# Performance work log

Hardware: AMD Instinct MI355X
Metric: run time of the kernel (lower is better)

Reference implementation:

```python
import jax, jax.numpy as jnp
import numpy as np

N = 600          # total nodes in episode
C = 5            # num_classes_output
Q = 16           # query_size
NQ = C * Q       # 80 query nodes (last rows)
F_IN = (1024, 1024)
EMB = (128, 128)
FE = 256         # final_embed_size
K = 3            # conv1d kernel
ST = 1           # conv1d stride
CAT = sum(EMB) + C            # 261
FC = FE + (FE - K) // ST + 1  # 510


def _edges():
    per = (N - NQ) // C
    labels = np.concatenate([np.repeat(np.arange(C), per), np.repeat(np.arange(C), Q)]).astype(np.int64)
    temp = labels.copy()
    temp[-NQ:] = -np.arange(1, NQ + 1)  # queries get unique pseudo-labels
    same = temp[:, None] == temp[None, :]
    eye = np.eye(N, dtype=bool)
    in_src, in_dst = np.nonzero(same & ~eye)        # in-class edges
    cr_src, cr_dst = np.nonzero(~same)              # cross-class edges
    q = np.arange(N - NQ, N); s = np.arange(N - NQ)
    a = np.repeat(q, s.size); b = np.tile(s, q.size)
    fin_src = np.concatenate([a, b]); fin_dst = np.concatenate([b, a])  # query<->support pooling
    f = lambda x: jnp.asarray(x, jnp.int32)
    return f(labels), f(in_src), f(in_dst), f(cr_src), f(cr_dst), f(fin_src), f(fin_dst)


def gcn(x, W, b, src, dst):
    # PyG GCNConv: add self-loops, D^-1/2 (A+I) D^-1/2 (X W) + b
    n = x.shape[0]
    loop = jnp.arange(n, dtype=src.dtype)
    s = jnp.concatenate([src, loop]); d = jnp.concatenate([dst, loop])
    deg = jax.ops.segment_sum(jnp.ones(s.shape, x.dtype), d, num_segments=n)
    dinv = jax.lax.rsqrt(deg)  # deg >= 1 (self-loops)
    norm = dinv[s] * dinv[d]
    h = x @ W
    return jax.ops.segment_sum(h[s] * norm[:, None], d, num_segments=n) + b


def gatv2(x, Wl, bl, Wr, br, att, b, src, dst):
    # PyG GATv2Conv (heads=1): e_ji = a . leaky_relu(hl[j] + hr[i]); out_i = sum_j softmax(e)_ji * hl[j]
    n = x.shape[0]
    loop = jnp.arange(n, dtype=src.dtype)
    s = jnp.concatenate([src, loop]); d = jnp.concatenate([dst, loop])
    hl = x @ Wl + bl
    hr = x @ Wr + br
    e = jax.nn.leaky_relu(hl[s] + hr[d], negative_slope=0.2) @ att  # [E]
    m = jax.ops.segment_max(e, d, num_segments=n)
    ex = jnp.exp(e - m[d])
    den = jax.ops.segment_sum(ex, d, num_segments=n)
    alpha = ex / den[d]
    return jax.ops.segment_sum(alpha[:, None] * hl[s], d, num_segments=n) + b


def setup_inputs() -> dict:
    key = jax.random.key(0)
    ks = jax.random.split(key, 12)
    labels, in_src, in_dst, cr_src, cr_dst, fin_src, fin_dst = _edges()
    p = lambda k, shp: jax.random.normal(k, shp, jnp.float32) * 0.05
    z = lambda shp: jnp.zeros(shp, jnp.float32)
    return {
        'features0': jax.random.normal(ks[0], (N, F_IN[0]), jnp.float32),
        'features1': jax.random.normal(ks[1], (N, F_IN[1]), jnp.float32),
        'labels': labels,
        'in_src': in_src, 'in_dst': in_dst,
        'cr_src': cr_src, 'cr_dst': cr_dst,
        'fin_src': fin_src, 'fin_dst': fin_dst,
        'W_f0': p(ks[2], (F_IN[0], EMB[0])), 'b_f0': z((EMB[0],)),
        'W_f1': p(ks[3], (F_IN[1], EMB[1])), 'b_f1': z((EMB[1],)),
        'W_in': p(ks[4], (CAT, FE)), 'b_in': z((FE,)),
        'Wl': p(ks[5], (CAT, FE)), 'bl': z((FE,)),
        'Wr': p(ks[6], (CAT, FE)), 'br': z((FE,)),
        'att_a': p(ks[7], (FE,)), 'b_gat': z((FE,)),
        'conv_w': p(ks[8], (1, 1, K)), 'conv_b': z((1,)),
        'W_lab': p(ks[9], (FC, C)), 'b_lab': z((C,)),
    }


def reference(features0, features1, labels, in_src, in_dst, cr_src, cr_dst, fin_src, fin_dst,
              W_f0, b_f0, W_f1, b_f1, W_in, b_in, Wl, bl, Wr, br, att_a, b_gat,
              conv_w, conv_b, W_lab, b_lab):
    ns = N - NQ
    one_hot = jnp.concatenate([
        jax.nn.one_hot(labels[:ns], C, dtype=jnp.float32),
        jnp.full((NQ, C), 1.0 / C, jnp.float32)], axis=0)
    # per-feature GCN embeddings (dropout = identity at inference)
    h0 = jax.nn.leaky_relu(gcn(features0, W_f0, b_f0, in_src, in_dst))
    h1 = jax.nn.leaky_relu(gcn(features1, W_f1, b_f1, in_src, in_dst))
    cated = jnp.concatenate([h0, h1, one_hot], axis=-1)  # [N, 261]
    gcn_emb = jax.nn.leaky_relu(gcn(cated, W_in, b_in, in_src, in_dst))          # [N, FE]
    gat_emb = jax.nn.elu(gatv2(cated, Wl, bl, Wr, br, att_a, b_gat, cr_src, cr_dst))  # [N, FE]
    conv = jax.lax.conv_general_dilated(gat_emb[:, None, :], conv_w, (ST,), 'VALID',
                                        dimension_numbers=('NCH', 'OIH', 'NCH'))
    gat_emb = jax.nn.sigmoid(conv[:, 0, :] + conv_b[0])  # [N, FE-K+1]
    fc = jnp.concatenate([gcn_emb, gat_emb], axis=-1)    # [N, FC]
    return gcn(fc, W_lab, b_lab, fin_src, fin_dst)       # [N, C]
```

## Files before the change

### kernel.cpp

```cpp
#include <hip/hip_runtime.h>

#define N_NODES 600
#define NSUP    520
#define NQ      80
#define C_CLS   5
#define PER     104
#define F_IN    1024
#define EMBF    128
#define FE      256
#define CATD    261
#define CST     264
#define FCD     510
#define CONV_OUT 254
#define R85     85

__global__ __launch_bounds__(1024) void k1_k(const float* __restrict__ f0,
                                             const float* __restrict__ f1,
                                             const float* __restrict__ Wf0,
                                             const float* __restrict__ Wf1,
                                             const float* __restrict__ bf0,
                                             const float* __restrict__ bf1,
                                             const float* __restrict__ Win,
                                             const float* __restrict__ Wl,
                                             const float* __restrict__ Wr,
                                             float* __restrict__ embp,
                                             float* __restrict__ xrow85,
                                             int* __restrict__ ctr) {
    __shared__ float xs[F_IN];
    __shared__ float part[1024];
    const int gb = blockIdx.x, t = threadIdx.x;
    if (gb == 0 && t == 0) *ctr = 0;
    if (gb < 40) {
        const int js  = gb & 3;
        const int c   = (gb >> 2) % C_CLS;
        const int set = gb / 20;
        const float* X = set ? f1 : f0;
        const float* W = set ? Wf1 : Wf0;
        const float* p = X + (size_t)(c * PER + js * 26) * F_IN + t;
        float acc = 0.f;
        for (int b = 0; b < 2; ++b) {
            float wv[13];
#pragma unroll
            for (int i = 0; i < 13; ++i) wv[i] = p[(size_t)(b * 13 + i) * F_IN];
#pragma unroll
            for (int i = 0; i < 13; ++i) acc += wv[i];
        }
        xs[t] = acc;
        __syncthreads();
        const int col = t & 127, kseg = t >> 7;
        const float* Wp = W + (size_t)(kseg * 128) * EMBF + col;
        const float* xp = xs + kseg * 128;
        float pacc = 0.f;
        for (int b = 0; b < 4; ++b) {
            float wv[32];
#pragma unroll
            for (int i = 0; i < 32; ++i) wv[i] = Wp[(size_t)(b * 32 + i) * EMBF];
#pragma unroll
            for (int i = 0; i < 32; ++i) pacc += xp[b * 32 + i] * wv[i];
        }
        part[t] = pacc;
        __syncthreads();
        if (t < 128) {
            float s = 0.f;
#pragma unroll
            for (int j = 0; j < 8; ++j) s += part[t + 128 * j];
            embp[((size_t)(set * 4 + js) * C_CLS + c) * EMBF + t] = s;
        }
    } else if (gb < 200) {
        const int idx = gb - 40, q = idx >> 1, set = idx & 1;
        const float* X = set ? f1 : f0;
        const float* W = set ? Wf1 : Wf0;
        if (t < 256) ((float4*)xs)[t] = ((const float4*)(X + (size_t)(NSUP + q) * F_IN))[t];
        __syncthreads();
        const int col = t & 127, kseg = t >> 7;
        const float* Wp = W + (size_t)(kseg * 128) * EMBF + col;
        const float* xp = xs + kseg * 128;
        float acc = 0.f;
        for (int b = 0; b < 4; ++b) {
            float wv[32];
#pragma unroll
            for (int i = 0; i < 32; ++i) wv[i] = Wp[(size_t)(b * 32 + i) * EMBF];
#pragma unroll
            for (int i = 0; i < 32; ++i) acc += xp[b * 32 + i] * wv[i];
        }
        part[t] = acc;
        __syncthreads();
        const int r = C_CLS + q;
        if (t < 128) {
            float s = 0.f;
#pragma unroll
            for (int j = 0; j < 8; ++j) s += part[t + 128 * j];
            s += (set ? bf1[t] : bf0[t]);
            s = s > 0.f ? s : 0.01f * s;
            xrow85[r * CST + set * EMBF + t] = s;
        }
        if (set == 0 && t < C_CLS) xrow85[r * CST + FE + t] = 0.2f;
    } else {
        const int wt = (gb - 200) * 1024 + t;
        float acc = 0.f;
        for (int i = wt; i < 16704 * 3; i += 16384) {
            const float4* p;
            int j = i;
            if (j < 16704) p = (const float4*)Win + j;
            else if ((j -= 16704) < 16704) p = (const float4*)Wl + j;
            else { j -= 16704; p = (const float4*)Wr + j; }
            float4 v = *p;
            acc += v.x + v.y + v.z + v.w;
        }
        asm volatile("" :: "v"(acc));
    }
}

__global__ __launch_bounds__(1024) void k2_k(const float* __restrict__ xrow85,
                                             const float* __restrict__ embp,
                                             const float* __restrict__ bf0,
                                             const float* __restrict__ bf1,
                                             const float* __restrict__ Win,
                                             const float* __restrict__ bin,
                                             const float* __restrict__ Wl,
                                             const float* __restrict__ bl,
                                             const float* __restrict__ Wr,
                                             const float* __restrict__ br,
                                             float* __restrict__ gcnA,
                                             float* __restrict__ hl85,
                                             float* __restrict__ hr85) {
    __shared__ float xrow[CATD + 3];
    __shared__ float part[1024];
    const int r = blockIdx.x, mat = blockIdx.y, t = threadIdx.x;
    if (r < C_CLS) {
        if (t < 256) {
            const int set = t >> 7, col = t & 127;
            float s = 0.f;
#pragma unroll
            for (int js = 0; js < 4; ++js)
                s += embp[((size_t)(set * 4 + js) * C_CLS + r) * EMBF + col];
            s = s * (1.f / PER) + (set ? bf1[col] : bf0[col]);
            s = s > 0.f ? s : 0.01f * s;
            xrow[set * 128 + col] = s;
        }
        if (t < C_CLS) xrow[FE + t] = (t == r) ? 1.f : 0.f;
    } else {
        if (t < CATD) xrow[t] = xrow85[r * CST + t];
    }
    __syncthreads();
    const float* W = (mat == 0) ? Win : (mat == 1 ? Wl : Wr);
    const float* B = (mat == 0) ? bin : (mat == 1 ? bl : br);
    const int col = t & 255, kq = t >> 8;
    const int k0 = kq * 65, k1 = (kq == 3) ? CATD : (kq + 1) * 65;
    const float* Wp = W + col;
    float acc = 0.f;
    int k = k0;
    for (; k + 32 <= k1; k += 32) {
        float wv[32];
#pragma unroll
        for (int i = 0; i < 32; ++i) wv[i] = Wp[(size_t)(k + i) * FE];
#pragma unroll
        for (int i = 0; i < 32; ++i) acc += xrow[k + i] * wv[i];
    }
    for (; k < k1; ++k) acc += xrow[k] * Wp[(size_t)k * FE];
    part[t] = acc;
    __syncthreads();
    if (t < 256) {
        float v = part[t] + part[t + 256] + part[t + 512] + part[t + 768] + B[t];
        if (mat == 0) { v = v > 0.f ? v : 0.01f * v; gcnA[r * FE + t] = v; }
        else if (mat == 1) hl85[r * FE + t] = v;
        else              hr85[r * FE + t] = v;
    }
}

__global__ __launch_bounds__(512) void gatfin_k(
    const float* __restrict__ hl85, const float* __restrict__ hr85,
    const float* __restrict__ att,  const float* __restrict__ bgat,
    const float* __restrict__ cw,   const float* __restrict__ cb,
    const float* __restrict__ gcnA, const float* __restrict__ Wlab,
    const float* __restrict__ blab,
    float* __restrict__ hlab, int* __restrict__ ctr, float* __restrict__ out) {
    __shared__ float es[R85 + 3], wsm[R85 + 3], go[FE], fcB[CONV_OUT + 2];
    __shared__ float part2[512], red[2], hpart[8][C_CLS];
    __shared__ float sS[C_CLS], sQ[C_CLS];
    __shared__ int flag;
    const int ir = blockIdx.x, t = threadIdx.x;
    const int lane = t & 63, w = t >> 6;

    float hrv[4], av[4];
#pragma unroll
    for (int p = 0; p < 4; ++p) {
        hrv[p] = hr85[ir * FE + p * 64 + lane];
        av[p]  = att[p * 64 + lane];
    }
    for (int jr = w; jr < R85; jr += 8) {
        float s = 0.f;
#pragma unroll
        for (int p = 0; p < 4; ++p) {
            float x = hl85[jr * FE + p * 64 + lane] + hrv[p];
            x = x > 0.f ? x : 0.2f * x;
            s += x * av[p];
        }
#pragma unroll
        for (int off = 32; off; off >>= 1) s += __shfl_xor(s, off);
        if (lane == 0) es[jr] = s;
    }
    __syncthreads();
    if (t < 64) {
        float m = es[t];
        if (t + 64 < R85) m = fmaxf(m, es[t + 64]);
#pragma unroll
        for (int off = 32; off; off >>= 1) m = fmaxf(m, __shfl_xor(m, off));
        if (t == 0) red[0] = m;
    }
    __syncthreads();
    const float m = red[0];
    if (t < R85) {
        float n;
        if (ir < C_CLS) n = (t < C_CLS) ? (t == ir ? 1.f : 104.f) : 1.f;
        else            n = (t < C_CLS) ? 104.f : 1.f;
        wsm[t] = n * __expf(es[t] - m);
    }
    __syncthreads();
    if (t < 64) {
        float d = wsm[t] + ((t + 64 < R85) ? wsm[t + 64] : 0.f);
#pragma unroll
        for (int off = 32; off; off >>= 1) d += __shfl_xor(d, off);
        if (t == 0) red[1] = 1.f / d;
    }
    __syncthreads();
    const float inv = red[1];
    {
        const int f = t & 255, half = t >> 8;
        const int j0 = half ? 43 : 0, j1 = half ? R85 : 43;
        float acc = 0.f;
        int jr = j0;
        for (; jr + 8 <= j1; jr += 8) {
            float wv[8];
#pragma unroll
            for (int i = 0; i < 8; ++i) wv[i] = hl85[(jr + i) * FE + f];
#pragma unroll
            for (int i = 0; i < 8; ++i) acc += wsm[jr + i] * wv[i];
        }
        for (; jr < j1; ++jr) acc += wsm[jr] * hl85[jr * FE + f];
        part2[t] = acc;
    }
    __syncthreads();
    if (t < FE) {
        float v = (part2[t] + part2[256 + t]) * inv + bgat[t];
        v = v > 0.f ? v : (__expf(v) - 1.f);
        go[t] = v;
    }
    __syncthreads();
    if (t < CONV_OUT)
        fcB[t] = 1.f / (1.f + __expf(-(go[t] * cw[0] + go[t + 1] * cw[1]
                                       + go[t + 2] * cw[2] + cb[0])));
    __syncthreads();
    {
        float a[C_CLS] = {0.f, 0.f, 0.f, 0.f, 0.f};
        if (t < FCD) {
            const float x = (t < FE) ? gcnA[ir * FE + t] : fcB[t - FE];
            const float* wl = Wlab + (size_t)t * C_CLS;
#pragma unroll
            for (int j = 0; j < C_CLS; ++j) a[j] = x * wl[j];
        }
#pragma unroll
        for (int j = 0; j < C_CLS; ++j) {
#pragma unroll
            for (int off = 32; off; off >>= 1) a[j] += __shfl_xor(a[j], off);
        }
        if (lane == 0) {
#pragma unroll
            for (int j = 0; j < C_CLS; ++j) hpart[w][j] = a[j];
        }
    }
    __syncthreads();
    if (t < C_CLS) {
        float s = 0.f;
#pragma unroll
        for (int ww = 0; ww < 8; ++ww) s += hpart[ww][t];
        hlab[ir * C_CLS + t] = s;
    }
    __syncthreads();
    __threadfence();
    if (t == 0) flag = (atomicAdd(ctr, 1) == R85 - 1) ? 1 : 0;
    __syncthreads();
    if (flag) {
        __threadfence();
        if (t < C_CLS) {
            float s = 0.f;
            for (int cl = 0; cl < C_CLS; ++cl) s += hlab[cl * C_CLS + t];
            sS[t] = 104.f * s;
        } else if (t < 2 * C_CLS) {
            const int c = t - C_CLS;
            float s = 0.f;
            for (int q = 0; q < NQ; ++q) s += hlab[(C_CLS + q) * C_CLS + c];
            sQ[c] = s;
        }
        __syncthreads();
        const float rs = rsqrtf(81.f * 521.f);
        for (int idx = t; idx < N_NODES * C_CLS; idx += 512) {
            const int i = idx / C_CLS, c = idx - i * C_CLS;
            float v;
            if (i < NSUP) v = sQ[c] * rs + hlab[(i / PER) * C_CLS + c] * (1.0f / 81.0f);
            else          v = sS[c] * rs + hlab[(C_CLS + i - NSUP) * C_CLS + c] * (1.0f / 521.0f);
            out[idx] = v + blab[c];
        }
        if (t == 0) *ctr = 0;
    }
}

extern "C" void kernel_launch(void* const* d_in, const int* in_sizes, int n_in,
                              void* d_out, int out_size, void* d_ws, size_t ws_size,
                              hipStream_t stream) {
    (void)in_sizes; (void)n_in; (void)out_size; (void)ws_size;
    const float* f0   = (const float*)d_in[0];
    const float* f1   = (const float*)d_in[1];
    const float* Wf0  = (const float*)d_in[9];
    const float* bf0  = (const float*)d_in[10];
    const float* Wf1  = (const float*)d_in[11];
    const float* bf1  = (const float*)d_in[12];
    const float* Win  = (const float*)d_in[13];
    const float* bin  = (const float*)d_in[14];
    const float* Wl   = (const float*)d_in[15];
    const float* bl   = (const float*)d_in[16];
    const float* Wr   = (const float*)d_in[17];
    const float* br   = (const float*)d_in[18];
    const float* att  = (const float*)d_in[19];
    const float* bgat = (const float*)d_in[20];
    const float* cw   = (const float*)d_in[21];
    const float* cb   = (const float*)d_in[22];
    const float* Wlab = (const float*)d_in[23];
    const float* blab = (const float*)d_in[24];
    float* out = (float*)d_out;

    float* ws = (float*)d_ws;
    float* gcnA   = ws;
    float* hl85   = ws + 21760;
    float* hr85   = ws + 43520;
    float* embp   = ws + 65280;
    float* xrow85 = ws + 70400;
    float* hlab   = ws + 92840;
    int*   ctr    = (int*)(ws + 93280);

    k1_k    <<<216, 1024, 0, stream>>>(f0, f1, Wf0, Wf1, bf0, bf1, Win, Wl, Wr,
                                       embp, xrow85, ctr);
    k2_k    <<<dim3(85, 3), 1024, 0, stream>>>(xrow85, embp, bf0, bf1,
                                               Win, bin, Wl, bl, Wr, br,
                                               gcnA, hl85, hr85);
    gatfin_k<<<85, 512, 0, stream>>>(hl85, hr85, att, bgat, cw, cb,
                                     gcnA, Wlab, blab, hlab, ctr, out);
}
```

Measured before the change: 42.30 us.

## Batch multiple rows per block in query embedding and k2 matmuls for weight reuse

Result: slower. 49.23 us (+16.4%).

```diff
diff --git a/kernel.cpp b/kernel.cpp
--- a/kernel.cpp
+++ b/kernel.cpp
@@ -26,8 +26,8 @@
                                              float* __restrict__ embp,
                                              float* __restrict__ xrow85,
                                              int* __restrict__ ctr) {
-    __shared__ float xs[F_IN];
-    __shared__ float part[1024];
+    __shared__ float xs[4 * F_IN];
+    __shared__ float part[4 * 1024];
     const int gb = blockIdx.x, t = threadIdx.x;
     if (gb == 0 && t == 0) *ctr = 0;
     if (gb < 40) {
@@ -66,37 +66,49 @@
             for (int j = 0; j < 8; ++j) s += part[t + 128 * j];
             embp[((size_t)(set * 4 + js) * C_CLS + c) * EMBF + t] = s;
         }
-    } else if (gb < 200) {
-        const int idx = gb - 40, q = idx >> 1, set = idx & 1;
+    } else if (gb < 80) {
+        const int idx = gb - 40, set = idx & 1, qt = idx >> 1;
         const float* X = set ? f1 : f0;
         const float* W = set ? Wf1 : Wf0;
-        if (t < 256) ((float4*)xs)[t] = ((const float4*)(X + (size_t)(NSUP + q) * F_IN))[t];
+        {
+            const int qr = t >> 8, f4 = t & 255;
+            ((float4*)xs)[t] =
+                ((const float4*)(X + (size_t)(NSUP + qt * 4 + qr) * F_IN))[f4];
+        }
         __syncthreads();
         const int col = t & 127, kseg = t >> 7;
         const float* Wp = W + (size_t)(kseg * 128) * EMBF + col;
-        const float* xp = xs + kseg * 128;
-        float acc = 0.f;
+        const int kb = kseg * 128;
+        float acc[4] = {0.f, 0.f, 0.f, 0.f};
         for (int b = 0; b < 4; ++b) {
             float wv[32];
 #pragma unroll
             for (int i = 0; i < 32; ++i) wv[i] = Wp[(size_t)(b * 32 + i) * EMBF];
 #pragma unroll
-            for (int i = 0; i < 32; ++i) acc += xp[b * 32 + i] * wv[i];
-        }
-        part[t] = acc;
-        __syncthreads();
-        const int r = C_CLS + q;
-        if (t < 128) {
+            for (int i = 0; i < 32; ++i) {
+                const int kk = kb + b * 32 + i;
+#pragma unroll
+                for (int q = 0; q < 4; ++q) acc[q] += xs[q * F_IN + kk] * wv[i];
+            }
+        }
+#pragma unroll
+        for (int q = 0; q < 4; ++q) part[q * 1024 + t] = acc[q];
+        __syncthreads();
+        if (t < 512) {
+            const int q = t >> 7, col2 = t & 127;
             float s = 0.f;
 #pragma unroll
-            for (int j = 0; j < 8; ++j) s += part[t + 128 * j];
-            s += (set ? bf1[t] : bf0[t]);
+            for (int j = 0; j < 8; ++j) s += part[q * 1024 + col2 + 128 * j];
+            s += (set ? bf1[col2] : bf0[col2]);
             s = s > 0.f ? s : 0.01f * s;
-            xrow85[r * CST + set * EMBF + t] = s;
-        }
-        if (set == 0 && t < C_CLS) xrow85[r * CST + FE + t] = 0.2f;
+            xrow85[(C_CLS + qt * 4 + q) * CST + set * EMBF + col2] = s;
+        }
+        if (set == 0 && t < 4 * C_CLS) {
+            const int q = t / C_CLS, c = t % C_CLS;
+            xrow85[(C_CLS + qt * 4 + q) * CST + FE + c] = 0.2f;
+        }
     } else {
-        const int wt = (gb - 200) * 1024 + t;
+        const int wt = (gb - 80) * 1024 + t;
         float acc = 0.f;
         for (int i = wt; i < 16704 * 3; i += 16384) {
             const float4* p;
@@ -124,47 +136,66 @@
                                              float* __restrict__ gcnA,
                                              float* __restrict__ hl85,
                                              float* __restrict__ hr85) {
-    __shared__ float xrow[CATD + 3];
-    __shared__ float part[1024];
-    const int r = blockIdx.x, mat = blockIdx.y, t = threadIdx.x;
-    if (r < C_CLS) {
-        if (t < 256) {
-            const int set = t >> 7, col = t & 127;
-            float s = 0.f;
-#pragma unroll
-            for (int js = 0; js < 4; ++js)
-                s += embp[((size_t)(set * 4 + js) * C_CLS + r) * EMBF + col];
-            s = s * (1.f / PER) + (set ? bf1[col] : bf0[col]);
-            s = s > 0.f ? s : 0.01f * s;
-            xrow[set * 128 + col] = s;
-        }
-        if (t < C_CLS) xrow[FE + t] = (t == r) ? 1.f : 0.f;
-    } else {
-        if (t < CATD) xrow[t] = xrow85[r * CST + t];
+    __shared__ float xr[5][CATD + 3];
+    __shared__ float part[5][1024];
+    const int bx = blockIdx.x, mat = blockIdx.y, t = threadIdx.x;
+    const int r0 = bx * 5;
+    for (int e = t; e < 5 * 264; e += 1024) {
+        const int rl = e / 264, k = e - rl * 264;
+        if (k >= CATD) continue;
+        const int r = r0 + rl;
+        float v;
+        if (r < C_CLS) {
+            if (k < FE) {
+                const int set = k >> 7, col = k & 127;
+                float s = 0.f;
+#pragma unroll
+                for (int js = 0; js < 4; ++js)
+                    s += embp[((size_t)(set * 4 + js) * C_CLS + r) * EMBF + col];
+                s = s * (1.f / PER) + (set ? bf1[col] : bf0[col]);
+                v = s > 0.f ? s : 0.01f * s;
+            } else {
+                v = (k - FE == r) ? 1.f : 0.f;
+            }
+        } else {
+            v = xrow85[r * CST + k];
+        }
+        xr[rl][k] = v;
     }
     __syncthreads();
     const float* W = (mat == 0) ? Win : (mat == 1 ? Wl : Wr);
     const float* B = (mat == 0) ? bin : (mat == 1 ? bl : br);
     const int col = t & 255, kq = t >> 8;
-    const int k0 = kq * 65, k1 = (kq == 3) ? CATD : (kq + 1) * 65;
+    const int k0 = kq * 65, k1v = (kq == 3) ? CATD : (kq + 1) * 65;
     const float* Wp = W + col;
-    float acc = 0.f;
+    float acc[5] = {0.f, 0.f, 0.f, 0.f, 0.f};
     int k = k0;
-    for (; k + 32 <= k1; k += 32) {
+    for (; k + 32 <= k1v; k += 32) {
         float wv[32];
 #pragma unroll
         for (int i = 0; i < 32; ++i) wv[i] = Wp[(size_t)(k + i) * FE];
 #pragma unroll
-        for (int i = 0; i < 32; ++i) acc += xrow[k + i] * wv[i];
-    }
-    for (; k < k1; ++k) acc += xrow[k] * Wp[(size_t)k * FE];
-    part[t] = acc;
-    __syncthreads();
-    if (t < 256) {
-        float v = part[t] + part[t + 256] + part[t + 512] + part[t + 768] + B[t];
-        if (mat == 0) { v = v > 0.f ? v : 0.01f * v; gcnA[r * FE + t] = v; }
-        else if (mat == 1) hl85[r * FE + t] = v;
-        else              hr85[r * FE + t] = v;
+        for (int i = 0; i < 32; ++i) {
+#pragma unroll
+            for (int rl = 0; rl < 5; ++rl) acc[rl] += xr[rl][k + i] * wv[i];
+        }
+    }
+    for (; k < k1v; ++k) {
+        const float w = Wp[(size_t)k * FE];
+#pragma unroll
+        for (int rl = 0; rl < 5; ++rl) acc[rl] += xr[rl][k] * w;
+    }
+#pragma unroll
+    for (int rl = 0; rl < 5; ++rl) part[rl][t] = acc[rl];
+    __syncthreads();
+    for (int u = t; u < 5 * 256; u += 1024) {
+        const int rl = u >> 8, c2 = u & 255;
+        float v = part[rl][c2] + part[rl][c2 + 256] + part[rl][c2 + 512]
+                + part[rl][c2 + 768] + B[c2];
+        const int r = r0 + rl;
+        if (mat == 0) { v = v > 0.f ? v : 0.01f * v; gcnA[r * FE + c2] = v; }
+        else if (mat == 1) hl85[r * FE + c2] = v;
+        else               hr85[r * FE + c2] = v;
     }
 }
 
@@ -338,9 +369,9 @@
     float* hlab   = ws + 92840;
     int*   ctr    = (int*)(ws + 93280);
 
-    k1_k    <<<216, 1024, 0, stream>>>(f0, f1, Wf0, Wf1, bf0, bf1, Win, Wl, Wr,
-                                       embp, xrow85, ctr);
-    k2_k    <<<dim3(85, 3), 1024, 0, stream>>>(xrow85, embp, bf0, bf1,
+    k1_k    <<<96, 1024, 0, stream>>>(f0, f1, Wf0, Wf1, bf0, bf1, Win, Wl, Wr,
+                                      embp, xrow85, ctr);
+    k2_k    <<<dim3(17, 3), 1024, 0, stream>>>(xrow85, embp, bf0, bf1,
                                                Win, bin, Wl, bl, Wr, br,
                                                gcnA, hl85, hr85);
     gatfin_k<<<85, 512, 0, stream>>>(hl85, hr85, att, bgat, cw, cb,
```
